# Kernel tuning notes

Measured on AMD Instinct MI355X. Metric: run time of the kernel, lower is better.

The kernel has to match this reference:

```python
import jax, jax.numpy as jnp
import numpy as np

B, C = 512, 128


def setup_inputs() -> dict:
    key = jax.random.key(0)
    k1, k2, k3 = jax.random.split(key, 3)
    return {
        "predicts": jax.random.normal(k1, (B, C), dtype=jnp.float32),
        "labels": jax.random.randint(k2, (B,), 0, C),
        "sim_all": jax.random.uniform(k3, (C, C), dtype=jnp.float32),
        "epoch": 5,
        "T": jnp.float32(2.0),
        "mu": jnp.float32(1.0),
        "eta": jnp.float32(1.0),
    }


def _lcd(predicts, labels, sim_all, T, mu, eta, epoch):
    eps = 1e-6
    B_, C_ = predicts.shape
    p = jax.nn.softmax(predicts / T, axis=1)  # (B, C)
    onehot = jax.nn.one_hot(labels, C_, dtype=p.dtype)  # (B, C)

    # sim_batch histogram: for each sample whose top-1 prediction equals the
    # label, increment sim_batch[label, runner_up]. Vectorized scatter-add
    # replaces the per-sample Python loop of the original.
    order = jnp.argsort(-p, axis=1)  # descending sort indices, (B, C)
    hit = (labels == order[:, 0]) & (C_ > 1)  # (B,)
    sim_batch = jnp.zeros((C_, C_), p.dtype).at[labels, order[:, 1]].add(
        hit.astype(p.dtype))

    # Pairwise log-ratio tensor: term[c, a, b] = p[a,c] * log(p[a,c]/(p[b,c]+eps)+eps)
    # (equivalent to the chunk/repeat/stack/permute construction in torch).
    pa = p.T[:, :, None]  # (C, B, 1)
    pb = p.T[:, None, :]  # (C, 1, B)
    term = pa * jnp.log(pa / (pb + eps) + eps)  # (C, B, B)

    triu1 = jnp.triu(jnp.ones((B_, B_), bool), 1)  # strictly upper mask
    loss_ab = jnp.sum(jnp.where(triu1, term, 0.0), axis=0)  # (B, B)

    same = labels[:, None] == labels[None, :]  # (B, B)
    IC = jnp.sum(jnp.abs(loss_ab * same))

    # inter_parm[c,a,b] = (onehot[a,c] != onehot[b,c]) on the strict upper triangle
    inter = (onehot.T[:, :, None] != onehot.T[:, None, :]) & triu1  # (C, B, B)
    isc_ab = jnp.sum(jnp.where(inter, term, 0.0), axis=0)  # (B, B)

    sim_b_diag = jnp.triu(sim_all[labels[:, None], labels[None, :]])
    if epoch == 0 or C_ == 1:
        sim_b_diag = jnp.triu(jnp.ones((B_, B_), p.dtype))
    ISC = jnp.sum(jnp.abs(isc_ab * sim_b_diag))

    same_count = jnp.sum((triu1 & same).astype(p.dtype))
    diff_count = jnp.sum((triu1 & ~same).astype(p.dtype))
    IC = jnp.where(same_count != 0, IC / same_count, IC)
    ISC = jnp.where(diff_count != 0, ISC / diff_count, ISC)
    ISC = jnp.where(ISC != 0, (1.0 / (ISC + eps)) * mu, ISC)
    IC = IC * eta
    return IC + ISC, sim_batch


def reference(predicts, labels, sim_all, epoch, T, mu, eta):
    return _lcd(predicts, labels, sim_all, T, mu, eta, epoch)
```

## Files before the change

### kernel.cpp

```cpp
#include <hip/hip_runtime.h>

#define BB 512
#define CC 128
#define EPS 1e-6f
#define PAIRBLK 511

__device__ __forceinline__ int tri(int a) { return (a * (1023 - a)) >> 1; }

__global__ __launch_bounds__(256) void row_kernel(
    const float* __restrict__ predicts, const int* __restrict__ labels,
    const float* __restrict__ Tp,
    float2* __restrict__ pxl, float* __restrict__ lg,
    float4* __restrict__ rowdat, int* __restrict__ hits,
    float* __restrict__ sim_batch) {
    const int tid = threadIdx.x, lane = tid & 63;
    const int row = blockIdx.x * 4 + (tid >> 6);

    if (tid < 128) sim_batch[blockIdx.x * 128 + tid] = 0.0f;

    const float T = Tp[0];
    const float z0 = predicts[row * CC + lane] / T;
    const float z1 = predicts[row * CC + 64 + lane] / T;

    float m = fmaxf(z0, z1);
    for (int s = 32; s; s >>= 1) m = fmaxf(m, __shfl_xor(m, s, 64));
    const float e0 = expf(z0 - m), e1 = expf(z1 - m);
    float sum = e0 + e1;
    for (int s = 32; s; s >>= 1) sum += __shfl_xor(sum, s, 64);

    const float inv = 1.0f / sum, ls = logf(sum);
    const float p0 = e0 * inv, p1 = e1 * inv;
    const float lp0 = (z0 - m) - ls, lp1 = (z1 - m) - ls;
    const float lg0 = logf(p0 + EPS), lg1 = logf(p1 + EPS);
    const float x0 = p0 * lp0, x1 = p1 * lp1;

    pxl[row * CC + lane]      = make_float2(p0, x0);
    pxl[row * CC + 64 + lane] = make_float2(p1, x1);
    lg[row * CC + lane]      = lg0;
    lg[row * CC + 64 + lane] = lg1;

    float hs = x0 + x1;
    for (int s = 32; s; s >>= 1) hs += __shfl_xor(hs, s, 64);

    const int lbl = labels[row];
    if (lane == (lbl & 63)) {
        const bool hi = lbl >= 64;
        rowdat[row] = make_float4(hs, hi ? p1 : p0, hi ? x1 : x0, hi ? lg1 : lg0);
    }

    unsigned long long k0 =
        (((unsigned long long)__float_as_uint(p0)) << 32) | (unsigned)(127 - lane);
    unsigned long long k1 =
        (((unsigned long long)__float_as_uint(p1)) << 32) | (unsigned)(127 - (lane + 64));
    unsigned long long hi = k0 > k1 ? k0 : k1;
    unsigned long long lo = k0 > k1 ? k1 : k0;
    for (int s = 32; s; s >>= 1) {
        const unsigned long long ohi = __shfl_xor(hi, s, 64);
        const unsigned long long olo = __shfl_xor(lo, s, 64);
        const unsigned long long nhi = hi > ohi ? hi : ohi;
        const unsigned long long c1 = hi > ohi ? ohi : hi;
        const unsigned long long c2 = lo > olo ? lo : olo;
        lo = c1 > c2 ? c1 : c2;
        hi = nhi;
    }
    if (lane == 0) {
        const int i1 = 127 - (int)(hi & 0xFFFFFFFFu);
        const int i2 = 127 - (int)(lo & 0xFFFFFFFFu);
        hits[row] = (i1 == lbl) ? i2 : -1;
    }
}

__global__ __launch_bounds__(256) void pairs_kernel(
    const float2* __restrict__ pxl, const float* __restrict__ lg,
    const float4* __restrict__ rowdat, const int* __restrict__ labels,
    const float* __restrict__ sim_all, const int* __restrict__ epoch_p,
    double* __restrict__ partials) {
    const int tid = threadIdx.x, lane = tid & 63, bid = blockIdx.x;
    const int k = bid * 256 + tid;

    int a = (int)((1023.0 - sqrt(1046529.0 - 8.0 * (double)k)) * 0.5);
    if (a < 0) a = 0;
    while (tri(a + 1) <= k) ++a;
    while (tri(a) > k) --a;
    const int b = a + 1 + (k - tri(a));

    const int la = labels[a], lb = labels[b];
    const bool same = (la == lb);
    const float4 ra = rowdat[a];

    double ic = 0.0, isc = 0.0, scnt = 0.0, dcnt = 0.0;

    if (!same) {
        const float g = lg[b * CC + la];
        const float4 rb = rowdat[b];
        const float2 pa = pxl[a * CC + lb];
        const float t1 = ra.z - ra.y * g;
        const float t2 = pa.y - pa.x * rb.w;
        const float sim = (epoch_p[0] == 0) ? 1.0f : sim_all[la * CC + lb];
        isc = fabsf((t1 + t2) * sim);
        dcnt = 1.0;
    }

    unsigned long long msk = __ballot(same);
    while (msk) {
        const int src = __builtin_ctzll(msk);
        msk &= msk - 1;
        const int aa = __shfl(a, src, 64);
        const int bb = __shfl(b, src, 64);
        float dot = pxl[aa * CC + lane].x * lg[bb * CC + lane] +
                    pxl[aa * CC + 64 + lane].x * lg[bb * CC + 64 + lane];
        for (int s = 32; s; s >>= 1) dot += __shfl_xor(dot, s, 64);
        if (lane == src) { ic = fabs((double)ra.x - (double)dot); scnt = 1.0; }
    }

    __shared__ double sred[4][4];
    double vals[4] = {ic, isc, scnt, dcnt};
    #pragma unroll
    for (int q = 0; q < 4; ++q) {
        double v = vals[q];
        for (int s = 32; s; s >>= 1) v += __shfl_xor(v, s, 64);
        if (lane == 0) sred[tid >> 6][q] = v;
    }
    __syncthreads();
    if (tid < 4)
        partials[bid * 4 + tid] =
            sred[0][tid] + sred[1][tid] + sred[2][tid] + sred[3][tid];
}

__global__ __launch_bounds__(256) void finalize_kernel(
    const double* __restrict__ partials, const int* __restrict__ labels,
    const int* __restrict__ hits, const float* __restrict__ mu_p,
    const float* __restrict__ eta_p, float* __restrict__ out) {
    const int tid = threadIdx.x, lane = tid & 63;

    float* sb = out + 1;
    for (int r = tid; r < BB; r += 256) {
        const int h = hits[r];
        if (h >= 0) atomicAdd(&sb[labels[r] * CC + h], 1.0f);
    }

    double v0 = 0, v1 = 0, v2 = 0, v3 = 0;
    for (int i = tid; i < PAIRBLK; i += 256) {
        v0 += partials[i * 4 + 0];
        v1 += partials[i * 4 + 1];
        v2 += partials[i * 4 + 2];
        v3 += partials[i * 4 + 3];
    }
    for (int s = 32; s; s >>= 1) {
        v0 += __shfl_xor(v0, s, 64);
        v1 += __shfl_xor(v1, s, 64);
        v2 += __shfl_xor(v2, s, 64);
        v3 += __shfl_xor(v3, s, 64);
    }
    __shared__ double sred[4][4];
    if (lane == 0) {
        sred[tid >> 6][0] = v0; sred[tid >> 6][1] = v1;
        sred[tid >> 6][2] = v2; sred[tid >> 6][3] = v3;
    }
    __syncthreads();
    if (tid == 0) {
        double IC  = sred[0][0] + sred[1][0] + sred[2][0] + sred[3][0];
        double ISC = sred[0][1] + sred[1][1] + sred[2][1] + sred[3][1];
        const double sc = sred[0][2] + sred[1][2] + sred[2][2] + sred[3][2];
        const double dc = sred[0][3] + sred[1][3] + sred[2][3] + sred[3][3];
        if (sc != 0.0) IC = IC / sc;
        if (dc != 0.0) ISC = ISC / dc;
        if (ISC != 0.0) ISC = (1.0 / (ISC + (double)EPS)) * (double)mu_p[0];
        IC = IC * (double)eta_p[0];
        out[0] = (float)(IC + ISC);
    }
}

extern "C" void kernel_launch(void* const* d_in, const int* in_sizes, int n_in,
                              void* d_out, int out_size, void* d_ws, size_t ws_size,
                              hipStream_t stream) {
    const float* predicts = (const float*)d_in[0];
    const int*   labels   = (const int*)d_in[1];
    const float* sim_all  = (const float*)d_in[2];
    const int*   epoch    = (const int*)d_in[3];
    const float* T        = (const float*)d_in[4];
    const float* mu       = (const float*)d_in[5];
    const float* eta      = (const float*)d_in[6];

    float* out = (float*)d_out;

    char* ws = (char*)d_ws;
    float2* pxl     = (float2*)ws;   ws += BB * CC * sizeof(float2);
    float*  lg      = (float*)ws;    ws += BB * CC * sizeof(float);
    float4* rowdat  = (float4*)ws;   ws += BB * sizeof(float4);
    int*    hits    = (int*)ws;      ws += BB * sizeof(int);
    double* partials = (double*)ws;

    row_kernel<<<BB / 4, 256, 0, stream>>>(predicts, labels, T, pxl, lg, rowdat,
                                           hits, out + 1);
    pairs_kernel<<<PAIRBLK, 256, 0, stream>>>(pxl, lg, rowdat, labels, sim_all,
                                              epoch, partials);
    finalize_kernel<<<1, 256, 0, stream>>>(partials, labels, hits, mu, eta, out);
}
```

Before: 17.69 us.

## Fuse softmax row pass into tiled pair kernel with shared-memory row tiles

Merges the row softmax kernel and the pair kernel into one kernel over 136 upper-triangular 32x32 row-tile pairs. Each block recomputes softmax, log terms and per-row scalars for its two row groups into LDS, then evaluates its pairs from shared memory instead of global intermediates. This drops one kernel launch and the global round trip of the per-row arrays. In exchange each row's softmax is recomputed in many tiles, fewer blocks run, and zeroing of sim_batch moves into the single-block finalize kernel.

```diff
diff --git a/kernel.cpp b/kernel.cpp
--- a/kernel.cpp
+++ b/kernel.cpp
@@ -3,127 +3,150 @@
 #define BB 512
 #define CC 128
 #define EPS 1e-6f
-#define PAIRBLK 511
-
-__device__ __forceinline__ int tri(int a) { return (a * (1023 - a)) >> 1; }
-
-__global__ __launch_bounds__(256) void row_kernel(
+#define G 32
+#define NG 16
+#define NTILE 136
+#define LDP 129
+
+__device__ __forceinline__ int pr32(int r) { return (r * (63 - r)) >> 1; }
+
+__global__ __launch_bounds__(256) void tile_kernel(
     const float* __restrict__ predicts, const int* __restrict__ labels,
-    const float* __restrict__ Tp,
-    float2* __restrict__ pxl, float* __restrict__ lg,
-    float4* __restrict__ rowdat, int* __restrict__ hits,
-    float* __restrict__ sim_batch) {
-    const int tid = threadIdx.x, lane = tid & 63;
-    const int row = blockIdx.x * 4 + (tid >> 6);
-
-    if (tid < 128) sim_batch[blockIdx.x * 128 + tid] = 0.0f;
+    const float* __restrict__ Tp, const float* __restrict__ sim_all,
+    const int* __restrict__ epoch_p,
+    int* __restrict__ hits, double* __restrict__ partials) {
+
+    __shared__ float pI[G][LDP], xI[G][LDP], gJ[G][LDP];
+    __shared__ float wI[G], xwI[G], HI[G], gwJ[G];
+    __shared__ int   laI[G], laJ[G];
+    __shared__ double sred[4][4];
+
+    const int tid = threadIdx.x, lane = tid & 63, wid = tid >> 6;
+
+    int t = blockIdx.x, i = 0;
+    while (t >= NG - i) { t -= NG - i; ++i; }
+    const int j = i + t;
+    const bool diag = (i == j);
 
     const float T = Tp[0];
-    const float z0 = predicts[row * CC + lane] / T;
-    const float z1 = predicts[row * CC + 64 + lane] / T;
-
-    float m = fmaxf(z0, z1);
-    for (int s = 32; s; s >>= 1) m = fmaxf(m, __shfl_xor(m, s, 64));
-    const float e0 = expf(z0 - m), e1 = expf(z1 - m);
-    float sum = e0 + e1;
-    for (int s = 32; s; s >>= 1) sum += __shfl_xor(sum, s, 64);
-
-    const float inv = 1.0f / sum, ls = logf(sum);
-    const float p0 = e0 * inv, p1 = e1 * inv;
-    const float lp0 = (z0 - m) - ls, lp1 = (z1 - m) - ls;
-    const float lg0 = logf(p0 + EPS), lg1 = logf(p1 + EPS);
-    const float x0 = p0 * lp0, x1 = p1 * lp1;
-
-    pxl[row * CC + lane]      = make_float2(p0, x0);
-    pxl[row * CC + 64 + lane] = make_float2(p1, x1);
-    lg[row * CC + lane]      = lg0;
-    lg[row * CC + 64 + lane] = lg1;
-
-    float hs = x0 + x1;
-    for (int s = 32; s; s >>= 1) hs += __shfl_xor(hs, s, 64);
-
-    const int lbl = labels[row];
-    if (lane == (lbl & 63)) {
-        const bool hi = lbl >= 64;
-        rowdat[row] = make_float4(hs, hi ? p1 : p0, hi ? x1 : x0, hi ? lg1 : lg0);
-    }
-
-    unsigned long long k0 =
-        (((unsigned long long)__float_as_uint(p0)) << 32) | (unsigned)(127 - lane);
-    unsigned long long k1 =
-        (((unsigned long long)__float_as_uint(p1)) << 32) | (unsigned)(127 - (lane + 64));
-    unsigned long long hi = k0 > k1 ? k0 : k1;
-    unsigned long long lo = k0 > k1 ? k1 : k0;
-    for (int s = 32; s; s >>= 1) {
-        const unsigned long long ohi = __shfl_xor(hi, s, 64);
-        const unsigned long long olo = __shfl_xor(lo, s, 64);
-        const unsigned long long nhi = hi > ohi ? hi : ohi;
-        const unsigned long long c1 = hi > ohi ? ohi : hi;
-        const unsigned long long c2 = lo > olo ? lo : olo;
-        lo = c1 > c2 ? c1 : c2;
-        hi = nhi;
-    }
-    if (lane == 0) {
-        const int i1 = 127 - (int)(hi & 0xFFFFFFFFu);
-        const int i2 = 127 - (int)(lo & 0xFFFFFFFFu);
-        hits[row] = (i1 == lbl) ? i2 : -1;
-    }
-}
-
-__global__ __launch_bounds__(256) void pairs_kernel(
-    const float2* __restrict__ pxl, const float* __restrict__ lg,
-    const float4* __restrict__ rowdat, const int* __restrict__ labels,
-    const float* __restrict__ sim_all, const int* __restrict__ epoch_p,
-    double* __restrict__ partials) {
-    const int tid = threadIdx.x, lane = tid & 63, bid = blockIdx.x;
-    const int k = bid * 256 + tid;
-
-    int a = (int)((1023.0 - sqrt(1046529.0 - 8.0 * (double)k)) * 0.5);
-    if (a < 0) a = 0;
-    while (tri(a + 1) <= k) ++a;
-    while (tri(a) > k) --a;
-    const int b = a + 1 + (k - tri(a));
-
-    const int la = labels[a], lb = labels[b];
-    const bool same = (la == lb);
-    const float4 ra = rowdat[a];
-
-    double ic = 0.0, isc = 0.0, scnt = 0.0, dcnt = 0.0;
-
-    if (!same) {
-        const float g = lg[b * CC + la];
-        const float4 rb = rowdat[b];
-        const float2 pa = pxl[a * CC + lb];
-        const float t1 = ra.z - ra.y * g;
-        const float t2 = pa.y - pa.x * rb.w;
-        const float sim = (epoch_p[0] == 0) ? 1.0f : sim_all[la * CC + lb];
-        isc = fabsf((t1 + t2) * sim);
-        dcnt = 1.0;
-    }
-
-    unsigned long long msk = __ballot(same);
-    while (msk) {
-        const int src = __builtin_ctzll(msk);
-        msk &= msk - 1;
-        const int aa = __shfl(a, src, 64);
-        const int bb = __shfl(b, src, 64);
-        float dot = pxl[aa * CC + lane].x * lg[bb * CC + lane] +
-                    pxl[aa * CC + 64 + lane].x * lg[bb * CC + 64 + lane];
-        for (int s = 32; s; s >>= 1) dot += __shfl_xor(dot, s, 64);
-        if (lane == src) { ic = fabs((double)ra.x - (double)dot); scnt = 1.0; }
-    }
-
-    __shared__ double sred[4][4];
-    double vals[4] = {ic, isc, scnt, dcnt};
+
+    const int nslots = diag ? G : 2 * G;
+    for (int slot = wid; slot < nslots; slot += 4) {
+        const bool isI = (slot < G);
+        const int r = isI ? slot : slot - G;
+        const int row = (isI ? i : j) * G + r;
+
+        const float z0 = predicts[row * CC + lane] / T;
+        const float z1 = predicts[row * CC + 64 + lane] / T;
+        float m = fmaxf(z0, z1);
+        for (int s = 32; s; s >>= 1) m = fmaxf(m, __shfl_xor(m, s, 64));
+        const float e0 = expf(z0 - m), e1 = expf(z1 - m);
+        float sum = e0 + e1;
+        for (int s = 32; s; s >>= 1) sum += __shfl_xor(sum, s, 64);
+
+        const float inv = 1.0f / sum, ls = logf(sum);
+        const float p0 = e0 * inv, p1 = e1 * inv;
+        const float lp0 = (z0 - m) - ls, lp1 = (z1 - m) - ls;
+        const float lg0 = logf(p0 + EPS), lg1 = logf(p1 + EPS);
+        const float x0 = p0 * lp0, x1 = p1 * lp1;
+        const int lbl = labels[row];
+
+        if (isI) {
+            pI[r][lane] = p0; pI[r][64 + lane] = p1;
+            xI[r][lane] = x0; xI[r][64 + lane] = x1;
+            float hs = x0 + x1;
+            for (int s = 32; s; s >>= 1) hs += __shfl_xor(hs, s, 64);
+            if (lane == 0) { HI[r] = hs; laI[r] = lbl; }
+            if (lane == (lbl & 63)) {
+                const bool hi = lbl >= 64;
+                wI[r]  = hi ? p1 : p0;
+                xwI[r] = hi ? x1 : x0;
+            }
+        }
+        if (!isI || diag) {
+            gJ[r][lane] = lg0; gJ[r][64 + lane] = lg1;
+            if (lane == 0) laJ[r] = lbl;
+            if (lane == (lbl & 63)) gwJ[r] = (lbl >= 64) ? lg1 : lg0;
+        }
+        if (diag) {
+            unsigned long long k0 =
+                (((unsigned long long)__float_as_uint(p0)) << 32) | (unsigned)(127 - lane);
+            unsigned long long k1 =
+                (((unsigned long long)__float_as_uint(p1)) << 32) | (unsigned)(127 - (lane + 64));
+            unsigned long long hi = k0 > k1 ? k0 : k1;
+            unsigned long long lo = k0 > k1 ? k1 : k0;
+            for (int s = 32; s; s >>= 1) {
+                const unsigned long long ohi = __shfl_xor(hi, s, 64);
+                const unsigned long long olo = __shfl_xor(lo, s, 64);
+                const unsigned long long nhi = hi > ohi ? hi : ohi;
+                const unsigned long long c1 = hi > ohi ? ohi : hi;
+                const unsigned long long c2 = lo > olo ? lo : olo;
+                lo = c1 > c2 ? c1 : c2;
+                hi = nhi;
+            }
+            if (lane == 0) {
+                const int i1 = 127 - (int)(hi & 0xFFFFFFFFu);
+                const int i2 = 127 - (int)(lo & 0xFFFFFFFFu);
+                hits[row] = (i1 == lbl) ? i2 : -1;
+            }
+        }
+    }
+    __syncthreads();
+
+    const int ep = epoch_p[0];
+    double ic = 0.0, isc = 0.0;
+    int scnt = 0, dcnt = 0;
+
+    const int npair = diag ? (G * (G - 1) / 2) : (G * G);
+    const int iters = (npair + 255) >> 8;
+    for (int it = 0; it < iters; ++it) {
+        const int idx = it * 256 + tid;
+        const bool valid = idx < npair;
+        int r = 0, s = 0;
+        if (valid) {
+            if (!diag) { r = idx >> 5; s = idx & 31; }
+            else {
+                r = (int)((63.0f - sqrtf(3969.0f - 8.0f * (float)idx)) * 0.5f);
+                if (r < 0) r = 0; if (r > 30) r = 30;
+                while (r < 30 && pr32(r + 1) <= idx) ++r;
+                while (r > 0 && pr32(r) > idx) --r;
+                s = r + 1 + (idx - pr32(r));
+            }
+        }
+        const int la = laI[r], lb = laJ[s];
+        const bool same = valid && (la == lb);
+
+        if (valid && !same) {
+            const float t1 = xwI[r] - wI[r] * gJ[s][la];
+            const float t2 = xI[r][lb] - pI[r][lb] * gwJ[s];
+            const float sim = (ep == 0) ? 1.0f : sim_all[la * CC + lb];
+            isc += (double)fabsf((t1 + t2) * sim);
+            ++dcnt;
+        }
+
+        unsigned long long msk = __ballot(same);
+        while (msk) {
+            const int src = __builtin_ctzll(msk);
+            msk &= msk - 1;
+            const int rr = __shfl(r, src, 64);
+            const int ss = __shfl(s, src, 64);
+            float dot = pI[rr][lane] * gJ[ss][lane] +
+                        pI[rr][64 + lane] * gJ[ss][64 + lane];
+            for (int st = 32; st; st >>= 1) dot += __shfl_xor(dot, st, 64);
+            if (lane == src) { ic += fabs((double)HI[rr] - (double)dot); ++scnt; }
+        }
+    }
+
+    double vals[4] = {ic, isc, (double)scnt, (double)dcnt};
     #pragma unroll
     for (int q = 0; q < 4; ++q) {
         double v = vals[q];
         for (int s = 32; s; s >>= 1) v += __shfl_xor(v, s, 64);
-        if (lane == 0) sred[tid >> 6][q] = v;
+        if (lane == 0) sred[wid][q] = v;
     }
     __syncthreads();
     if (tid < 4)
-        partials[bid * 4 + tid] =
+        partials[blockIdx.x * 4 + tid] =
             sred[0][tid] + sred[1][tid] + sred[2][tid] + sred[3][tid];
 }
 
@@ -133,18 +156,19 @@
     const float* __restrict__ eta_p, float* __restrict__ out) {
     const int tid = threadIdx.x, lane = tid & 63;
 
-    float* sb = out + 1;
+    for (int idx = tid; idx < CC * CC; idx += 256) out[1 + idx] = 0.0f;
+    __syncthreads();
     for (int r = tid; r < BB; r += 256) {
         const int h = hits[r];
-        if (h >= 0) atomicAdd(&sb[labels[r] * CC + h], 1.0f);
+        if (h >= 0) atomicAdd(&out[1 + labels[r] * CC + h], 1.0f);
     }
 
     double v0 = 0, v1 = 0, v2 = 0, v3 = 0;
-    for (int i = tid; i < PAIRBLK; i += 256) {
-        v0 += partials[i * 4 + 0];
-        v1 += partials[i * 4 + 1];
-        v2 += partials[i * 4 + 2];
-        v3 += partials[i * 4 + 3];
+    for (int b = tid; b < NTILE; b += 256) {
+        v0 += partials[b * 4 + 0];
+        v1 += partials[b * 4 + 1];
+        v2 += partials[b * 4 + 2];
+        v3 += partials[b * 4 + 3];
     }
     for (int s = 32; s; s >>= 1) {
         v0 += __shfl_xor(v0, s, 64);
@@ -185,15 +209,11 @@
     float* out = (float*)d_out;
 
     char* ws = (char*)d_ws;
-    float2* pxl     = (float2*)ws;   ws += BB * CC * sizeof(float2);
-    float*  lg      = (float*)ws;    ws += BB * CC * sizeof(float);
-    float4* rowdat  = (float4*)ws;   ws += BB * sizeof(float4);
-    int*    hits    = (int*)ws;      ws += BB * sizeof(int);
+    int*    hits     = (int*)ws;      ws += BB * sizeof(int);
+    ws += (8 - ((size_t)ws & 7)) & 7;
     double* partials = (double*)ws;
 
-    row_kernel<<<BB / 4, 256, 0, stream>>>(predicts, labels, T, pxl, lg, rowdat,
-                                           hits, out + 1);
-    pairs_kernel<<<PAIRBLK, 256, 0, stream>>>(pxl, lg, rowdat, labels, sim_all,
-                                              epoch, partials);
+    tile_kernel<<<NTILE, 256, 0, stream>>>(predicts, labels, T, sim_all, epoch,
+                                           hits, partials);
     finalize_kernel<<<1, 256, 0, stream>>>(partials, labels, hits, mu, eta, out);
 }
```

Result: slower. 29.47 us (+66.6%).

## Fuse finalize into pairs kernel via last-block ticket; two pairs per thread

Applied to the files above, without the earlier changes.

The separate finalize kernel is removed. A global atomic ticket, reset in row_kernel, lets the last pairs block to finish do the sim_batch histogram and the final reduction. Each thread now handles two pairs, which halves the pairs grid to 256 blocks and the partials the final step must reduce. This saves one kernel launch and its dependency gap, at the cost of threadfence and atomic overhead and fewer, longer-running blocks.

```diff
diff --git a/kernel.cpp b/kernel.cpp
--- a/kernel.cpp
+++ b/kernel.cpp
@@ -3,7 +3,8 @@
 #define BB 512
 #define CC 128
 #define EPS 1e-6f
-#define PAIRBLK 511
+#define NPAIR 130816
+#define NPB 256
 
 __device__ __forceinline__ int tri(int a) { return (a * (1023 - a)) >> 1; }
 
@@ -12,11 +13,12 @@
     const float* __restrict__ Tp,
     float2* __restrict__ pxl, float* __restrict__ lg,
     float4* __restrict__ rowdat, int* __restrict__ hits,
-    float* __restrict__ sim_batch) {
+    float* __restrict__ sim_batch, unsigned int* __restrict__ ticket) {
     const int tid = threadIdx.x, lane = tid & 63;
     const int row = blockIdx.x * 4 + (tid >> 6);
 
     if (tid < 128) sim_batch[blockIdx.x * 128 + tid] = 0.0f;
+    if (blockIdx.x == 0 && tid == 0) *ticket = 0u;
 
     const float T = Tp[0];
     const float z0 = predicts[row * CC + lane] / T;
@@ -73,48 +75,90 @@
 __global__ __launch_bounds__(256) void pairs_kernel(
     const float2* __restrict__ pxl, const float* __restrict__ lg,
     const float4* __restrict__ rowdat, const int* __restrict__ labels,
-    const float* __restrict__ sim_all, const int* __restrict__ epoch_p,
-    double* __restrict__ partials) {
+    const int* __restrict__ hits, const float* __restrict__ sim_all,
+    const int* __restrict__ epoch_p, const float* __restrict__ mu_p,
+    const float* __restrict__ eta_p, double* __restrict__ partials,
+    unsigned int* __restrict__ ticket, float* __restrict__ out) {
     const int tid = threadIdx.x, lane = tid & 63, bid = blockIdx.x;
-    const int k = bid * 256 + tid;
-
-    int a = (int)((1023.0 - sqrt(1046529.0 - 8.0 * (double)k)) * 0.5);
-    if (a < 0) a = 0;
-    while (tri(a + 1) <= k) ++a;
-    while (tri(a) > k) --a;
-    const int b = a + 1 + (k - tri(a));
-
-    const int la = labels[a], lb = labels[b];
-    const bool same = (la == lb);
-    const float4 ra = rowdat[a];
-
-    double ic = 0.0, isc = 0.0, scnt = 0.0, dcnt = 0.0;
-
-    if (!same) {
-        const float g = lg[b * CC + la];
-        const float4 rb = rowdat[b];
-        const float2 pa = pxl[a * CC + lb];
-        const float t1 = ra.z - ra.y * g;
+    __shared__ double sred[4][4];
+    __shared__ int lastflag;
+
+    const int ep = epoch_p[0];
+    double ic = 0.0, isc = 0.0;
+    int scnt = 0, dcnt = 0;
+
+    const int k0 = bid * 256 + tid;
+    const int k1 = k0 + 65536;
+    const bool valid1 = k1 < NPAIR;
+
+    int a0 = (int)((1023.0 - sqrt(1046529.0 - 8.0 * (double)k0)) * 0.5);
+    if (a0 < 0) a0 = 0;
+    while (tri(a0 + 1) <= k0) ++a0;
+    while (tri(a0) > k0) --a0;
+    const int b0 = a0 + 1 + (k0 - tri(a0));
+
+    int a1 = 0, b1 = 1;
+    if (valid1) {
+        a1 = (int)((1023.0 - sqrt(1046529.0 - 8.0 * (double)k1)) * 0.5);
+        if (a1 < 0) a1 = 0;
+        while (tri(a1 + 1) <= k1) ++a1;
+        while (tri(a1) > k1) --a1;
+        b1 = a1 + 1 + (k1 - tri(a1));
+    }
+
+    const int la0 = labels[a0], lb0 = labels[b0];
+    const int la1 = labels[a1], lb1 = labels[b1];
+    const bool same0 = (la0 == lb0);
+    const bool same1 = valid1 && (la1 == lb1);
+
+    const float4 ra0 = rowdat[a0];
+    const float4 ra1 = rowdat[a1];
+
+    if (!same0) {
+        const float g  = lg[b0 * CC + la0];
+        const float4 rb = rowdat[b0];
+        const float2 pa = pxl[a0 * CC + lb0];
+        const float t1 = ra0.z - ra0.y * g;
         const float t2 = pa.y - pa.x * rb.w;
-        const float sim = (epoch_p[0] == 0) ? 1.0f : sim_all[la * CC + lb];
-        isc = fabsf((t1 + t2) * sim);
-        dcnt = 1.0;
-    }
-
-    unsigned long long msk = __ballot(same);
+        const float sim = (ep == 0) ? 1.0f : sim_all[la0 * CC + lb0];
+        isc += (double)fabsf((t1 + t2) * sim);
+        ++dcnt;
+    }
+    if (valid1 && !same1) {
+        const float g  = lg[b1 * CC + la1];
+        const float4 rb = rowdat[b1];
+        const float2 pa = pxl[a1 * CC + lb1];
+        const float t1 = ra1.z - ra1.y * g;
+        const float t2 = pa.y - pa.x * rb.w;
+        const float sim = (ep == 0) ? 1.0f : sim_all[la1 * CC + lb1];
+        isc += (double)fabsf((t1 + t2) * sim);
+        ++dcnt;
+    }
+
+    unsigned long long msk = __ballot(same0);
     while (msk) {
         const int src = __builtin_ctzll(msk);
         msk &= msk - 1;
-        const int aa = __shfl(a, src, 64);
-        const int bb = __shfl(b, src, 64);
+        const int aa = __shfl(a0, src, 64);
+        const int bb = __shfl(b0, src, 64);
         float dot = pxl[aa * CC + lane].x * lg[bb * CC + lane] +
                     pxl[aa * CC + 64 + lane].x * lg[bb * CC + 64 + lane];
         for (int s = 32; s; s >>= 1) dot += __shfl_xor(dot, s, 64);
-        if (lane == src) { ic = fabs((double)ra.x - (double)dot); scnt = 1.0; }
-    }
-
-    __shared__ double sred[4][4];
-    double vals[4] = {ic, isc, scnt, dcnt};
+        if (lane == src) { ic += fabs((double)ra0.x - (double)dot); ++scnt; }
+    }
+    msk = __ballot(same1);
+    while (msk) {
+        const int src = __builtin_ctzll(msk);
+        msk &= msk - 1;
+        const int aa = __shfl(a1, src, 64);
+        const int bb = __shfl(b1, src, 64);
+        float dot = pxl[aa * CC + lane].x * lg[bb * CC + lane] +
+                    pxl[aa * CC + 64 + lane].x * lg[bb * CC + 64 + lane];
+        for (int s = 32; s; s >>= 1) dot += __shfl_xor(dot, s, 64);
+        if (lane == src) { ic += fabs((double)ra1.x - (double)dot); ++scnt; }
+    }
+
+    double vals[4] = {ic, isc, (double)scnt, (double)dcnt};
     #pragma unroll
     for (int q = 0; q < 4; ++q) {
         double v = vals[q];
@@ -125,49 +169,47 @@
     if (tid < 4)
         partials[bid * 4 + tid] =
             sred[0][tid] + sred[1][tid] + sred[2][tid] + sred[3][tid];
-}
-
-__global__ __launch_bounds__(256) void finalize_kernel(
-    const double* __restrict__ partials, const int* __restrict__ labels,
-    const int* __restrict__ hits, const float* __restrict__ mu_p,
-    const float* __restrict__ eta_p, float* __restrict__ out) {
-    const int tid = threadIdx.x, lane = tid & 63;
-
-    float* sb = out + 1;
-    for (int r = tid; r < BB; r += 256) {
-        const int h = hits[r];
-        if (h >= 0) atomicAdd(&sb[labels[r] * CC + h], 1.0f);
-    }
-
-    double v0 = 0, v1 = 0, v2 = 0, v3 = 0;
-    for (int i = tid; i < PAIRBLK; i += 256) {
-        v0 += partials[i * 4 + 0];
-        v1 += partials[i * 4 + 1];
-        v2 += partials[i * 4 + 2];
-        v3 += partials[i * 4 + 3];
-    }
-    for (int s = 32; s; s >>= 1) {
-        v0 += __shfl_xor(v0, s, 64);
-        v1 += __shfl_xor(v1, s, 64);
-        v2 += __shfl_xor(v2, s, 64);
-        v3 += __shfl_xor(v3, s, 64);
-    }
-    __shared__ double sred[4][4];
-    if (lane == 0) {
-        sred[tid >> 6][0] = v0; sred[tid >> 6][1] = v1;
-        sred[tid >> 6][2] = v2; sred[tid >> 6][3] = v3;
-    }
+
     __syncthreads();
     if (tid == 0) {
-        double IC  = sred[0][0] + sred[1][0] + sred[2][0] + sred[3][0];
-        double ISC = sred[0][1] + sred[1][1] + sred[2][1] + sred[3][1];
-        const double sc = sred[0][2] + sred[1][2] + sred[2][2] + sred[3][2];
-        const double dc = sred[0][3] + sred[1][3] + sred[2][3] + sred[3][3];
-        if (sc != 0.0) IC = IC / sc;
-        if (dc != 0.0) ISC = ISC / dc;
-        if (ISC != 0.0) ISC = (1.0 / (ISC + (double)EPS)) * (double)mu_p[0];
-        IC = IC * (double)eta_p[0];
-        out[0] = (float)(IC + ISC);
+        __threadfence();
+        const unsigned old = atomicAdd(ticket, 1u);
+        lastflag = (old == NPB - 1) ? 1 : 0;
+    }
+    __syncthreads();
+    if (lastflag) {
+        __threadfence();
+        for (int r = tid; r < BB; r += 256) {
+            const int h = hits[r];
+            if (h >= 0) atomicAdd(&out[1 + labels[r] * CC + h], 1.0f);
+        }
+        double v0 = partials[tid * 4 + 0];
+        double v1 = partials[tid * 4 + 1];
+        double v2 = partials[tid * 4 + 2];
+        double v3 = partials[tid * 4 + 3];
+        for (int s = 32; s; s >>= 1) {
+            v0 += __shfl_xor(v0, s, 64);
+            v1 += __shfl_xor(v1, s, 64);
+            v2 += __shfl_xor(v2, s, 64);
+            v3 += __shfl_xor(v3, s, 64);
+        }
+        if (lane == 0) {
+            sred[tid >> 6][0] = v0; sred[tid >> 6][1] = v1;
+            sred[tid >> 6][2] = v2; sred[tid >> 6][3] = v3;
+        }
+        __syncthreads();
+        if (tid == 0) {
+            double IC  = sred[0][0] + sred[1][0] + sred[2][0] + sred[3][0];
+            double ISC = sred[0][1] + sred[1][1] + sred[2][1] + sred[3][1];
+            const double sc = sred[0][2] + sred[1][2] + sred[2][2] + sred[3][2];
+            const double dc = sred[0][3] + sred[1][3] + sred[2][3] + sred[3][3];
+            if (sc != 0.0) IC = IC / sc;
+            if (dc != 0.0) ISC = ISC / dc;
+            if (ISC != 0.0) ISC = (1.0 / (ISC + (double)EPS)) * (double)mu_p[0];
+            IC = IC * (double)eta_p[0];
+            out[0] = (float)(IC + ISC);
+            *ticket = 0u;
+        }
     }
 }
 
@@ -189,11 +231,11 @@
     float*  lg      = (float*)ws;    ws += BB * CC * sizeof(float);
     float4* rowdat  = (float4*)ws;   ws += BB * sizeof(float4);
     int*    hits    = (int*)ws;      ws += BB * sizeof(int);
-    double* partials = (double*)ws;
+    double* partials = (double*)ws;  ws += NPB * 4 * sizeof(double);
+    unsigned int* ticket = (unsigned int*)ws;
 
     row_kernel<<<BB / 4, 256, 0, stream>>>(predicts, labels, T, pxl, lg, rowdat,
-                                           hits, out + 1);
-    pairs_kernel<<<PAIRBLK, 256, 0, stream>>>(pxl, lg, rowdat, labels, sim_all,
-                                              epoch, partials);
-    finalize_kernel<<<1, 256, 0, stream>>>(partials, labels, hits, mu, eta, out);
+                                           hits, out + 1, ticket);
+    pairs_kernel<<<NPB, 256, 0, stream>>>(pxl, lg, rowdat, labels, hits, sim_all,
+                                          epoch, mu, eta, partials, ticket, out);
 }
```

Result: slower. 21.32 us (+20.5%).
